# Performance work log

Measured on AMD Instinct MI355X. Metric: run time of the kernel, lower is better.

## Reference

```python
import jax, jax.numpy as jnp
import numpy as np

B, T, D = 4, 1024, 1024
NEXP, TOPK = 8, 2
N = B * T
# eval capacity: floor(TOPK * 2.0 * N / NEXP) = 2048, already even and >= min_capacity
CAP = 2048
LN_EPS = 1e-5


def setup_inputs() -> dict:
    key = jax.random.key(0)
    ks = jax.random.split(key, 4)
    x = jax.random.normal(ks[0], (B, T, D), jnp.float32)
    w_g = jax.random.normal(ks[1], (D, NEXP), jnp.float32) * 0.02
    c_fc = jax.random.normal(ks[2], (NEXP, D, 4 * D), jnp.float32) * 0.02
    c_proj = jax.random.normal(ks[3], (NEXP, 4 * D, D), jnp.float32) * 0.02
    ln_w = jnp.ones((D,), jnp.float32)
    ln_b = jnp.zeros((D,), jnp.float32)
    return {"x": x, "w_g": w_g, "c_fc": c_fc, "c_proj": c_proj, "ln_w": ln_w, "ln_b": ln_b}


def moe_forward(x, w_g, c_fc, c_proj, ln_w, ln_b):
    xf = x.reshape(N, D)
    # --- Router ---
    logits = xf @ w_g                                   # [N, E]
    topk_vals, topk_idx = jax.lax.top_k(logits, TOPK)   # [N, K]
    masked = jnp.full_like(logits, -jnp.inf)
    masked = masked.at[jnp.arange(N)[:, None], topk_idx].set(topk_vals)
    probs = jax.nn.softmax(masked, axis=-1)             # [N, E]

    # capacity-based ranking (slot 0 for all tokens first, then slot 1, ...)
    onehot = jax.nn.one_hot(topk_idx, NEXP, dtype=jnp.int32)     # [N, K, E]
    exp_mask = jnp.transpose(onehot, (1, 0, 2))                  # [K, N, E]
    rank = jnp.cumsum(exp_mask.reshape(TOPK * N, NEXP), axis=0) - 1
    rank = rank.reshape(TOPK, N, NEXP)
    exp_mask = exp_mask * (rank < CAP).astype(jnp.int32)         # drop overflow
    rank_tok = jnp.sum(exp_mask * rank, axis=-1)                 # [K, N]
    exp_w = exp_mask.astype(probs.dtype) * probs[None]           # [K, N, E]
    rank_oh = jax.nn.one_hot(rank_tok, CAP, dtype=probs.dtype)   # [K, N, C]
    cb_weight = jnp.einsum('kne,knc->nec', exp_w, rank_oh)       # [N, E, C]
    sec_mask = (cb_weight != 0).astype(x.dtype)                  # dispatch mask

    # --- dispatch -> experts -> combine ---
    xb = jnp.einsum('nec,nd->ecd', sec_mask, xf)                 # [E, C, D]
    h = jax.nn.gelu(jnp.einsum('ecd,edf->ecf', xb, c_fc), approximate=False)
    eo = jnp.einsum('ecf,efd->ecd', h, c_proj)                   # [E, C, D]
    out = jnp.einsum('nec,ecd->nd', cb_weight, eo)               # [N, D]

    # --- LayerNorm ---
    mu = out.mean(-1, keepdims=True)
    var = out.var(-1, keepdims=True)
    out = (out - mu) / jnp.sqrt(var + LN_EPS) * ln_w + ln_b
    return out.reshape(B, T, D)


def reference(x, w_g, c_fc, c_proj, ln_w, ln_b):
    return moe_forward(x, w_g, c_fc, c_proj, ln_w, ln_b)
```

## Files before the change

kernel.cpp:

```cpp
#include <hip/hip_runtime.h>
#include <math.h>

#define NEXP 8
#define CAP 2048
#define NTOK 4096
#define DDIM 1024
#define FDIM 4096

typedef __bf16 bf16x8 __attribute__((ext_vector_type(8)));
typedef float f32x4 __attribute__((ext_vector_type(4)));
typedef unsigned short u16x8 __attribute__((ext_vector_type(8)));

__device__ __forceinline__ unsigned short f2bf(float f) {
    unsigned int u = __float_as_uint(f);
    u += 0x7FFFu + ((u >> 16) & 1u);
    return (unsigned short)(u >> 16);
}

__device__ __forceinline__ void gld_lds16(const void* g, void* l) {
    __builtin_amdgcn_global_load_lds((const __attribute__((address_space(1))) void*)g,
                                     (__attribute__((address_space(3))) void*)l, 16, 0, 0);
}

__global__ __launch_bounds__(256) void transpose_cvt64(const float* __restrict__ in,
                                                       unsigned short* __restrict__ out,
                                                       int R, int C) {
    __shared__ float tile[64][65];
    int e = blockIdx.z;
    const float* ip = in + (size_t)e * R * C;
    unsigned short* op = out + (size_t)e * R * C;
    int c0 = blockIdx.x * 64, r0 = blockIdx.y * 64;
    int t = threadIdx.x;
#pragma unroll
    for (int i = 0; i < 4; i++) {
        int rr = i * 16 + (t >> 4);
        int cc = (t & 15) * 4;
        float4 v = *(const float4*)&ip[(size_t)(r0 + rr) * C + c0 + cc];
        tile[rr][cc] = v.x; tile[rr][cc + 1] = v.y; tile[rr][cc + 2] = v.z; tile[rr][cc + 3] = v.w;
    }
    __syncthreads();
    int c = t >> 2, rb = (t & 3) * 16;
    u16x8 o0, o1;
#pragma unroll
    for (int j = 0; j < 8; j++) o0[j] = f2bf(tile[rb + j][c]);
#pragma unroll
    for (int j = 0; j < 8; j++) o1[j] = f2bf(tile[rb + 8 + j][c]);
    unsigned short* dst = op + (size_t)(c0 + c) * R + r0 + rb;
    *(u16x8*)dst = o0;
    *(u16x8*)(dst + 8) = o1;
}

__global__ __launch_bounds__(256) void router_kernel(const float* __restrict__ x,
                                                     const float* __restrict__ wg,
                                                     int2* __restrict__ e01,
                                                     float2* __restrict__ p01) {
    int wid = threadIdx.x >> 6, lane = threadIdx.x & 63;
    int n = blockIdx.x * 4 + wid;
    float acc[8];
#pragma unroll
    for (int i = 0; i < 8; i++) acc[i] = 0.f;
    const float4* xr = (const float4*)(x + (size_t)n * DDIM);
#pragma unroll
    for (int j = 0; j < 4; j++) {
        float4 xv = xr[j * 64 + lane];
        int base = (j * 64 + lane) * 4;
        float xs[4] = {xv.x, xv.y, xv.z, xv.w};
#pragma unroll
        for (int t = 0; t < 4; t++) {
            const float4* wr = (const float4*)(wg + (size_t)(base + t) * 8);
            float4 w0 = wr[0], w1 = wr[1];
            acc[0] += xs[t] * w0.x; acc[1] += xs[t] * w0.y;
            acc[2] += xs[t] * w0.z; acc[3] += xs[t] * w0.w;
            acc[4] += xs[t] * w1.x; acc[5] += xs[t] * w1.y;
            acc[6] += xs[t] * w1.z; acc[7] += xs[t] * w1.w;
        }
    }
#pragma unroll
    for (int off = 32; off > 0; off >>= 1) {
#pragma unroll
        for (int i = 0; i < 8; i++) acc[i] += __shfl_xor(acc[i], off);
    }
    if (lane == 0) {
        int i0 = 0; float v0 = acc[0];
#pragma unroll
        for (int q = 1; q < 8; q++) { if (acc[q] > v0) { v0 = acc[q]; i0 = q; } }
        int i1 = -1; float v1 = -3.0e38f;
#pragma unroll
        for (int q = 0; q < 8; q++) { if (q != i0 && acc[q] > v1) { v1 = acc[q]; i1 = q; } }
        float ea = expf(v0 - v0), eb = expf(v1 - v0);
        float inv = 1.f / (ea + eb);
        e01[n] = make_int2(i0, i1);
        p01[n] = make_float2(ea * inv, eb * inv);
    }
}

__global__ void assign_kernel(const int2* __restrict__ e01, int* __restrict__ counts,
                              int* __restrict__ assign_row, int* __restrict__ tok_slot) {
    int lane = threadIdx.x;
    int base[8];
#pragma unroll
    for (int i = 0; i < 8; i++) base[i] = 0;
    unsigned long long below = ((unsigned long long)1 << lane) - 1ull;
    int2 cur = e01[lane];
    for (int pass = 0; pass < 2; ++pass) {
        for (int t = 0; t < NTOK; t += 64) {
            int n = t + lane;
            int2 nxt;
            if (t + 64 < NTOK) nxt = e01[t + 64 + lane];
            else nxt = (pass == 0) ? e01[lane] : make_int2(0, 0);
            int ex = (pass == 0) ? cur.x : cur.y;
            int slot = -1;
#pragma unroll
            for (int q = 0; q < 8; q++) {
                unsigned long long m = __ballot(ex == q);
                if (ex == q) slot = base[q] + __popcll(m & below);
                base[q] += __popcll(m);
            }
            if (slot < CAP) {
                assign_row[ex * CAP + slot] = n;
                tok_slot[2 * n + pass] = slot;
            } else {
                tok_slot[2 * n + pass] = -1;
            }
            cur = nxt;
        }
    }
    if (lane < 8) counts[lane] = base[lane] > CAP ? CAP : base[lane];
}

__global__ __launch_bounds__(256) void gather_rows(const float* __restrict__ x,
                                                   const int* __restrict__ assign_row,
                                                   const int* __restrict__ counts,
                                                   unsigned short* __restrict__ xg) {
    int e = blockIdx.y;
    int wid = threadIdx.x >> 6, lane = threadIdx.x & 63;
    int slot = blockIdx.x * 4 + wid;
    if (slot >= counts[e]) return;
    int n = assign_row[e * CAP + slot];
    const float4* src = (const float4*)(x + (size_t)n * DDIM);
    unsigned short* dst = xg + ((size_t)e * CAP + slot) * DDIM;
#pragma unroll
    for (int j = 0; j < 4; j++) {
        float4 v = src[j * 64 + lane];
        ushort4 o;
        o.x = f2bf(v.x); o.y = f2bf(v.y); o.z = f2bf(v.z); o.w = f2bf(v.w);
        *(ushort4*)(dst + (size_t)(j * 64 + lane) * 4) = o;
    }
}

template <bool GELU>
__global__ __launch_bounds__(512, 2) void gemm_pipe(const unsigned short* __restrict__ A,
                                                    const unsigned short* __restrict__ Bt,
                                                    void* __restrict__ Cout,
                                                    const int* __restrict__ counts,
                                                    int Mcap, int Ncols, int K) {
    constexpr int ABYTES = 128 * 64 * 2;
    constexpr int BBYTES = 256 * 64 * 2;
    constexpr int BUFB = ABYTES + BBYTES;
    __shared__ __align__(16) char smem[3 * BUFB];

    int gx = gridDim.x, gy = gridDim.y;
    int nwg = gx * gy * gridDim.z;
    int flat = blockIdx.x + gx * (blockIdx.y + gy * blockIdx.z);
    int cpx = nwg >> 3;
    int swz = (flat & 7) * cpx + (flat >> 3);
    int gxy = gx * gy;
    int e  = swz / gxy;
    int r2 = swz - e * gxy;
    int by = r2 / gx;
    int bx = r2 - by * gx;

    int cnt = counts[e];
    int row0 = by * 128;
    if (row0 >= cnt) return;
    int col0 = bx * 256;

    int tid = threadIdx.x;
    int w = tid >> 6, lane = tid & 63;
    int wm = w >> 2, wn = w & 3;

    const unsigned short* Ab = A + ((size_t)e * Mcap + row0) * K;
    const unsigned short* Bb = Bt + ((size_t)e * Ncols + col0) * K;
    int NT = K >> 6;

    int srow = w * 8 + (lane >> 3);
    int sElem = ((lane & 7) ^ (lane >> 3)) * 8;
    int ldst = w * 1024 + lane * 16;

    int a_off[4][2], b_off[4][2];
#pragma unroll
    for (int m = 0; m < 4; m++) {
        int row = wm * 64 + m * 16 + (lane & 15);
#pragma unroll
        for (int ks = 0; ks < 2; ks++) {
            int j = ks * 4 + (lane >> 4);
            a_off[m][ks] = row * 128 + ((j ^ (row & 7)) * 16);
        }
    }
#pragma unroll
    for (int n = 0; n < 4; n++) {
        int row = wn * 64 + n * 16 + (lane & 15);
#pragma unroll
        for (int ks = 0; ks < 2; ks++) {
            int j = ks * 4 + (lane >> 4);
            b_off[n][ks] = row * 128 + ((j ^ (row & 7)) * 16);
        }
    }

    auto stage = [&](int tt) {
        int bb = (tt % 3) * BUFB;
        size_t kq = (size_t)tt * 64 + sElem;
#pragma unroll
        for (int r = 0; r < 2; r++)
            gld_lds16(Ab + (size_t)(r * 64 + srow) * K + kq, smem + bb + r * 8192 + ldst);
#pragma unroll
        for (int r = 0; r < 4; r++)
            gld_lds16(Bb + (size_t)(r * 64 + srow) * K + kq, smem + bb + ABYTES + r * 8192 + ldst);
    };

    f32x4 acc[4][4] = {};

    stage(0); stage(1);
    asm volatile("s_waitcnt vmcnt(6)" ::: "memory");
    __builtin_amdgcn_sched_barrier(0);
    __builtin_amdgcn_s_barrier();

    for (int t = 0; t < NT; ++t) {
        const int bb = (t % 3) * BUFB;
        bf16x8 af[4][2], bf[4][2];
#pragma unroll
        for (int m = 0; m < 4; m++)
#pragma unroll
            for (int ks = 0; ks < 2; ks++)
                af[m][ks] = *(const bf16x8*)(smem + bb + a_off[m][ks]);
#pragma unroll
        for (int n = 0; n < 4; n++)
#pragma unroll
            for (int ks = 0; ks < 2; ks++)
                bf[n][ks] = *(const bf16x8*)(smem + bb + ABYTES + b_off[n][ks]);

        if (t + 2 < NT) stage(t + 2);

        if (t + 1 < NT) {
            if (t + 2 < NT) asm volatile("s_waitcnt vmcnt(6)" ::: "memory");
            else            asm volatile("s_waitcnt vmcnt(0)" ::: "memory");
        }
        __builtin_amdgcn_sched_barrier(0);
        __builtin_amdgcn_s_barrier();
        asm volatile("s_waitcnt lgkmcnt(0)" ::: "memory");
        __builtin_amdgcn_sched_barrier(0);

        __builtin_amdgcn_s_setprio(1);
#pragma unroll
        for (int ks = 0; ks < 2; ks++)
#pragma unroll
            for (int m = 0; m < 4; m++)
#pragma unroll
                for (int n = 0; n < 4; n++)
                    acc[m][n] = __builtin_amdgcn_mfma_f32_16x16x32_bf16(af[m][ks], bf[n][ks], acc[m][n], 0, 0, 0);
        __builtin_amdgcn_s_setprio(0);
        __builtin_amdgcn_s_barrier();
    }

    unsigned short* Cb_h = (unsigned short*)Cout + ((size_t)e * Mcap + row0) * Ncols + col0;
    float* Cb_f = (float*)Cout + ((size_t)e * Mcap + row0) * Ncols + col0;
#pragma unroll
    for (int m = 0; m < 4; m++)
#pragma unroll
        for (int n = 0; n < 4; n++)
#pragma unroll
            for (int j = 0; j < 4; j++) {
                int lr = wm * 64 + m * 16 + ((lane >> 4) << 2) + j;
                int lc = wn * 64 + n * 16 + (lane & 15);
                float v = acc[m][n][j];
                if constexpr (GELU) {
                    float g = 0.5f * v * (1.0f + erff(v * 0.70710678118654752f));
                    Cb_h[(size_t)lr * Ncols + lc] = f2bf(g);
                } else {
                    Cb_f[(size_t)lr * Ncols + lc] = v;
                }
            }
}

__global__ __launch_bounds__(256) void combine_ln_kernel(const float* __restrict__ eo,
                                                         const int2* __restrict__ e01,
                                                         const float2* __restrict__ p01,
                                                         const int* __restrict__ tok_slot,
                                                         const float* __restrict__ lnw,
                                                         const float* __restrict__ lnb,
                                                         float* __restrict__ out) {
    int n = blockIdx.x, t = threadIdx.x;
    int2 e = e01[n];
    float2 p = p01[n];
    int s0 = tok_slot[2 * n], s1 = tok_slot[2 * n + 1];
    float o0 = 0.f, o1 = 0.f, o2 = 0.f, o3 = 0.f;
    if (s0 >= 0) {
        const float4* r = (const float4*)(eo + ((size_t)e.x * CAP + s0) * DDIM);
        float4 v = r[t];
        o0 += p.x * v.x; o1 += p.x * v.y; o2 += p.x * v.z; o3 += p.x * v.w;
    }
    if (s1 >= 0) {
        const float4* r = (const float4*)(eo + ((size_t)e.y * CAP + s1) * DDIM);
        float4 v = r[t];
        o0 += p.y * v.x; o1 += p.y * v.y; o2 += p.y * v.z; o3 += p.y * v.w;
    }
    float s = o0 + o1 + o2 + o3;
    float sq = o0 * o0 + o1 * o1 + o2 * o2 + o3 * o3;
#pragma unroll
    for (int off = 32; off > 0; off >>= 1) {
        s += __shfl_xor(s, off);
        sq += __shfl_xor(sq, off);
    }
    __shared__ float red[8];
    int wid = t >> 6, lane = t & 63;
    if (lane == 0) { red[wid] = s; red[4 + wid] = sq; }
    __syncthreads();
    s = red[0] + red[1] + red[2] + red[3];
    sq = red[4] + red[5] + red[6] + red[7];
    float mu = s * (1.f / DDIM);
    float var = sq * (1.f / DDIM) - mu * mu;
    float inv = rsqrtf(var + 1e-5f);
    const float4 w = ((const float4*)lnw)[t];
    const float4 b = ((const float4*)lnb)[t];
    float4 r;
    r.x = (o0 - mu) * inv * w.x + b.x;
    r.y = (o1 - mu) * inv * w.y + b.y;
    r.z = (o2 - mu) * inv * w.z + b.z;
    r.w = (o3 - mu) * inv * w.w + b.w;
    ((float4*)(out + (size_t)n * DDIM))[t] = r;
}

extern "C" void kernel_launch(void* const* d_in, const int* in_sizes, int n_in,
                              void* d_out, int out_size, void* d_ws, size_t ws_size,
                              hipStream_t stream) {
    const float* x   = (const float*)d_in[0];
    const float* wg  = (const float*)d_in[1];
    const float* cfc = (const float*)d_in[2];
    const float* cpr = (const float*)d_in[3];
    const float* lnw = (const float*)d_in[4];
    const float* lnb = (const float*)d_in[5];
    float* out = (float*)d_out;

    char* ws = (char*)d_ws;
    size_t off = 0;
    auto take = [&](size_t b) {
        char* p = ws + off;
        off += (b + 255) & ~(size_t)255;
        return p;
    };
    unsigned short* cfct = (unsigned short*)take((size_t)NEXP * FDIM * DDIM * 2);
    float* eo = (float*)cfct;
    unsigned short* cprt = (unsigned short*)take((size_t)NEXP * DDIM * FDIM * 2);
    unsigned short* xg   = (unsigned short*)take((size_t)NEXP * CAP * DDIM * 2);
    unsigned short* h    = (unsigned short*)take((size_t)NEXP * CAP * FDIM * 2);
    int2*   e01      = (int2*)take(NTOK * sizeof(int2));
    float2* p01      = (float2*)take(NTOK * sizeof(float2));
    int*    tok_slot = (int*)take((size_t)NTOK * 2 * 4);
    int*    assign_row = (int*)take((size_t)NEXP * CAP * 4);
    int*    counts   = (int*)take(256);

    transpose_cvt64<<<dim3(FDIM / 64, DDIM / 64, NEXP), 256, 0, stream>>>(cfc, cfct, DDIM, FDIM);
    transpose_cvt64<<<dim3(DDIM / 64, FDIM / 64, NEXP), 256, 0, stream>>>(cpr, cprt, FDIM, DDIM);
    router_kernel<<<NTOK / 4, 256, 0, stream>>>(x, wg, e01, p01);
    assign_kernel<<<1, 64, 0, stream>>>(e01, counts, assign_row, tok_slot);
    gather_rows<<<dim3(CAP / 4, NEXP), 256, 0, stream>>>(x, assign_row, counts, xg);
    gemm_pipe<true ><<<dim3(FDIM / 256, CAP / 128, NEXP), 512, 0, stream>>>(xg, cfct, (void*)h, counts, CAP, FDIM, DDIM);
    gemm_pipe<false><<<dim3(DDIM / 256, CAP / 128, NEXP), 512, 0, stream>>>(h, cprt, (void*)eo, counts, CAP, DDIM, FDIM);
    combine_ln_kernel<<<NTOK, 256, 0, stream>>>(eo, e01, p01, tok_slot, lnw, lnb, out);
}
```

Before: 415.9 us.

## Template expert GEMM with two-phase K-step pipeline and per-GEMM tile shapes

Replaces the fixed 128x256 triple-buffered expert GEMM with a templated kernel that uses K-steps of 32, four LDS buffers, and splits each step into two half-M MFMA phases. The A and B tile loads are staged separately between the phases. The FC GEMM now uses 256x256 tiles and the projection GEMM uses 256x128 tiles. The aim is better overlap of global-to-LDS loads with MFMA work and more operand reuse per workgroup. In exchange it adds barriers per K-step, raises register and LDS pressure, and launches fewer workgroups for the FC GEMM.

```diff
diff --git a/kernel.cpp b/kernel.cpp
--- a/kernel.cpp
+++ b/kernel.cpp
@@ -148,16 +148,23 @@
     }
 }
 
-template <bool GELU>
-__global__ __launch_bounds__(512, 2) void gemm_pipe(const unsigned short* __restrict__ A,
-                                                    const unsigned short* __restrict__ Bt,
-                                                    void* __restrict__ Cout,
-                                                    const int* __restrict__ counts,
-                                                    int Mcap, int Ncols, int K) {
-    constexpr int ABYTES = 128 * 64 * 2;
-    constexpr int BBYTES = 256 * 64 * 2;
+template <int WGN, int MF, int NF, bool GELU>
+__global__ __launch_bounds__(512, 2) void gemm_2ph(const unsigned short* __restrict__ A,
+                                                   const unsigned short* __restrict__ Bt,
+                                                   void* __restrict__ Cout,
+                                                   const int* __restrict__ counts,
+                                                   int Mcap, int Ncols, int K) {
+    constexpr int WGM = 8 / WGN;
+    constexpr int BM = WGM * MF * 16;
+    constexpr int BN = WGN * NF * 16;
+    constexpr int ABYTES = BM * 64;
+    constexpr int BBYTES = BN * 64;
     constexpr int BUFB = ABYTES + BBYTES;
-    __shared__ __align__(16) char smem[3 * BUFB];
+    constexpr int GA = (BM * 4) / 512;
+    constexpr int GB = (BN * 4) / 512;
+    constexpr int LPT = GA + GB;
+    constexpr int MH = MF / 2;
+    __shared__ __align__(16) char smem[4 * BUFB];
 
     int gx = gridDim.x, gy = gridDim.y;
     int nwg = gx * gy * gridDim.z;
@@ -171,108 +178,119 @@
     int bx = r2 - by * gx;
 
     int cnt = counts[e];
-    int row0 = by * 128;
+    int row0 = by * BM;
     if (row0 >= cnt) return;
-    int col0 = bx * 256;
+    int col0 = bx * BN;
 
     int tid = threadIdx.x;
     int w = tid >> 6, lane = tid & 63;
-    int wm = w >> 2, wn = w & 3;
+    int wm = w / WGN, wn = w % WGN;
 
     const unsigned short* Ab = A + ((size_t)e * Mcap + row0) * K;
     const unsigned short* Bb = Bt + ((size_t)e * Ncols + col0) * K;
-    int NT = K >> 6;
-
-    int srow = w * 8 + (lane >> 3);
-    int sElem = ((lane & 7) ^ (lane >> 3)) * 8;
+    int NT = K >> 5;
+
+    int sAr[GA], sAk[GA], sBr[GB], sBk[GB];
+#pragma unroll
+    for (int i = 0; i < GA; i++) {
+        int c = i * 512 + tid, cp = c ^ ((c >> 4) & 3);
+        sAr[i] = cp >> 2; sAk[i] = (cp & 3) * 8;
+    }
+#pragma unroll
+    for (int i = 0; i < GB; i++) {
+        int c = i * 512 + tid, cp = c ^ ((c >> 4) & 3);
+        sBr[i] = cp >> 2; sBk[i] = (cp & 3) * 8;
+    }
     int ldst = w * 1024 + lane * 16;
 
-    int a_off[4][2], b_off[4][2];
-#pragma unroll
-    for (int m = 0; m < 4; m++) {
-        int row = wm * 64 + m * 16 + (lane & 15);
-#pragma unroll
-        for (int ks = 0; ks < 2; ks++) {
-            int j = ks * 4 + (lane >> 4);
-            a_off[m][ks] = row * 128 + ((j ^ (row & 7)) * 16);
-        }
-    }
-#pragma unroll
-    for (int n = 0; n < 4; n++) {
-        int row = wn * 64 + n * 16 + (lane & 15);
-#pragma unroll
-        for (int ks = 0; ks < 2; ks++) {
-            int j = ks * 4 + (lane >> 4);
-            b_off[n][ks] = row * 128 + ((j ^ (row & 7)) * 16);
-        }
-    }
-
-    auto stage = [&](int tt) {
-        int bb = (tt % 3) * BUFB;
-        size_t kq = (size_t)tt * 64 + sElem;
-#pragma unroll
-        for (int r = 0; r < 2; r++)
-            gld_lds16(Ab + (size_t)(r * 64 + srow) * K + kq, smem + bb + r * 8192 + ldst);
-#pragma unroll
-        for (int r = 0; r < 4; r++)
-            gld_lds16(Bb + (size_t)(r * 64 + srow) * K + kq, smem + bb + ABYTES + r * 8192 + ldst);
+    int a_off[MF], b_off[NF];
+    int j = lane >> 4;
+#pragma unroll
+    for (int m = 0; m < MF; m++) {
+        int row = wm * (MF * 16) + m * 16 + (lane & 15);
+        a_off[m] = row * 64 + ((j ^ ((row >> 2) & 3)) * 16);
+    }
+#pragma unroll
+    for (int n = 0; n < NF; n++) {
+        int row = wn * (NF * 16) + n * 16 + (lane & 15);
+        b_off[n] = row * 64 + ((j ^ ((row >> 2) & 3)) * 16);
+    }
+
+    auto stageA = [&](int tt) {
+        int bb = (tt & 3) * BUFB;
+        size_t kt = (size_t)tt * 32;
+#pragma unroll
+        for (int i = 0; i < GA; i++)
+            gld_lds16(Ab + (size_t)sAr[i] * K + kt + sAk[i], smem + bb + i * 8192 + ldst);
     };
-
-    f32x4 acc[4][4] = {};
-
-    stage(0); stage(1);
-    asm volatile("s_waitcnt vmcnt(6)" ::: "memory");
+    auto stageB = [&](int tt) {
+        int bb = (tt & 3) * BUFB + ABYTES;
+        size_t kt = (size_t)tt * 32;
+#pragma unroll
+        for (int i = 0; i < GB; i++)
+            gld_lds16(Bb + (size_t)sBr[i] * K + kt + sBk[i], smem + bb + i * 8192 + ldst);
+    };
+
+#define VM_LPT() do { if constexpr (LPT == 4) asm volatile("s_waitcnt vmcnt(4)" ::: "memory"); \
+                      else                    asm volatile("s_waitcnt vmcnt(3)" ::: "memory"); } while (0)
+
+    f32x4 acc[MF][NF] = {};
+
+    stageA(0); stageB(0); stageA(1); stageB(1);
+    VM_LPT();
     __builtin_amdgcn_sched_barrier(0);
     __builtin_amdgcn_s_barrier();
 
     for (int t = 0; t < NT; ++t) {
-        const int bb = (t % 3) * BUFB;
-        bf16x8 af[4][2], bf[4][2];
-#pragma unroll
-        for (int m = 0; m < 4; m++)
-#pragma unroll
-            for (int ks = 0; ks < 2; ks++)
-                af[m][ks] = *(const bf16x8*)(smem + bb + a_off[m][ks]);
-#pragma unroll
-        for (int n = 0; n < 4; n++)
-#pragma unroll
-            for (int ks = 0; ks < 2; ks++)
-                bf[n][ks] = *(const bf16x8*)(smem + bb + ABYTES + b_off[n][ks]);
-
-        if (t + 2 < NT) stage(t + 2);
-
-        if (t + 1 < NT) {
-            if (t + 2 < NT) asm volatile("s_waitcnt vmcnt(6)" ::: "memory");
-            else            asm volatile("s_waitcnt vmcnt(0)" ::: "memory");
-        }
+        const int bb = (t & 3) * BUFB;
+        bf16x8 af[MF], bfr[NF];
+#pragma unroll
+        for (int n = 0; n < NF; n++) bfr[n] = *(const bf16x8*)(smem + bb + ABYTES + b_off[n]);
+#pragma unroll
+        for (int m = 0; m < MH; m++) af[m] = *(const bf16x8*)(smem + bb + a_off[m]);
+        if (t + 2 < NT) stageA(t + 2);
+        __builtin_amdgcn_s_barrier();
+        asm volatile("s_waitcnt lgkmcnt(0)" ::: "memory");
+        __builtin_amdgcn_sched_barrier(0);
+        __builtin_amdgcn_s_setprio(1);
+#pragma unroll
+        for (int m = 0; m < MH; m++)
+#pragma unroll
+            for (int n = 0; n < NF; n++)
+                acc[m][n] = __builtin_amdgcn_mfma_f32_16x16x32_bf16(af[m], bfr[n], acc[m][n], 0, 0, 0);
+        __builtin_amdgcn_s_setprio(0);
+        __builtin_amdgcn_s_barrier();
+#pragma unroll
+        for (int m = MH; m < MF; m++) af[m] = *(const bf16x8*)(smem + bb + a_off[m]);
+        if (t + 2 < NT) stageB(t + 2);
+        if (t + 2 < NT)      VM_LPT();
+        else if (t + 1 < NT) asm volatile("s_waitcnt vmcnt(0)" ::: "memory");
         __builtin_amdgcn_sched_barrier(0);
         __builtin_amdgcn_s_barrier();
         asm volatile("s_waitcnt lgkmcnt(0)" ::: "memory");
         __builtin_amdgcn_sched_barrier(0);
-
         __builtin_amdgcn_s_setprio(1);
 #pragma unroll
-        for (int ks = 0; ks < 2; ks++)
-#pragma unroll
-            for (int m = 0; m < 4; m++)
-#pragma unroll
-                for (int n = 0; n < 4; n++)
-                    acc[m][n] = __builtin_amdgcn_mfma_f32_16x16x32_bf16(af[m][ks], bf[n][ks], acc[m][n], 0, 0, 0);
+        for (int m = MH; m < MF; m++)
+#pragma unroll
+            for (int n = 0; n < NF; n++)
+                acc[m][n] = __builtin_amdgcn_mfma_f32_16x16x32_bf16(af[m], bfr[n], acc[m][n], 0, 0, 0);
         __builtin_amdgcn_s_setprio(0);
         __builtin_amdgcn_s_barrier();
     }
+#undef VM_LPT
 
     unsigned short* Cb_h = (unsigned short*)Cout + ((size_t)e * Mcap + row0) * Ncols + col0;
     float* Cb_f = (float*)Cout + ((size_t)e * Mcap + row0) * Ncols + col0;
 #pragma unroll
-    for (int m = 0; m < 4; m++)
-#pragma unroll
-        for (int n = 0; n < 4; n++)
-#pragma unroll
-            for (int j = 0; j < 4; j++) {
-                int lr = wm * 64 + m * 16 + ((lane >> 4) << 2) + j;
-                int lc = wn * 64 + n * 16 + (lane & 15);
-                float v = acc[m][n][j];
+    for (int m = 0; m < MF; m++)
+#pragma unroll
+        for (int n = 0; n < NF; n++)
+#pragma unroll
+            for (int jj = 0; jj < 4; jj++) {
+                int lr = wm * (MF * 16) + m * 16 + ((lane >> 4) << 2) + jj;
+                int lc = wn * (NF * 16) + n * 16 + (lane & 15);
+                float v = acc[m][n][jj];
                 if constexpr (GELU) {
                     float g = 0.5f * v * (1.0f + erff(v * 0.70710678118654752f));
                     Cb_h[(size_t)lr * Ncols + lc] = f2bf(g);
@@ -364,7 +382,7 @@
     router_kernel<<<NTOK / 4, 256, 0, stream>>>(x, wg, e01, p01);
     assign_kernel<<<1, 64, 0, stream>>>(e01, counts, assign_row, tok_slot);
     gather_rows<<<dim3(CAP / 4, NEXP), 256, 0, stream>>>(x, assign_row, counts, xg);
-    gemm_pipe<true ><<<dim3(FDIM / 256, CAP / 128, NEXP), 512, 0, stream>>>(xg, cfct, (void*)h, counts, CAP, FDIM, DDIM);
-    gemm_pipe<false><<<dim3(DDIM / 256, CAP / 128, NEXP), 512, 0, stream>>>(h, cprt, (void*)eo, counts, CAP, DDIM, FDIM);
+    gemm_2ph<4, 8, 4, true ><<<dim3(FDIM / 256, CAP / 256, NEXP), 512, 0, stream>>>(xg, cfct, (void*)h, counts, CAP, FDIM, DDIM);
+    gemm_2ph<2, 4, 4, false><<<dim3(DDIM / 128, CAP / 256, NEXP), 512, 0, stream>>>(h, cprt, (void*)eo, counts, CAP, DDIM, FDIM);
     combine_ln_kernel<<<NTOK, 256, 0, stream>>>(eo, e01, p01, tok_slot, lnw, lnb, out);
 }
```

After: 443.9 us. 6.7% more time.

## Replace triple-buffered K64 GEMM with templated double-buffered K32 GEMM

Applied to the files above, without the earlier changes.

Swaps the 3-stage, 64-wide-K pipelined expert GEMM for a templated double-buffered kernel that uses 32-wide K tiles, a new LDS swizzle and a plain __syncthreads per iteration. The template lets the second GEMM run with 128x128 tiles and 256 threads, which gives more workgroups for the narrow N=1024 output. Launch bounds are raised to 4 waves per EU, trading pipeline depth for occupancy. The cost is a barrier every 32 K, half the MFMA work between barriers, and the loss of the explicit vmcnt-based overlap.

```diff
diff --git a/kernel.cpp b/kernel.cpp
--- a/kernel.cpp
+++ b/kernel.cpp
@@ -148,16 +148,21 @@
     }
 }
 
-template <bool GELU>
-__global__ __launch_bounds__(512, 2) void gemm_pipe(const unsigned short* __restrict__ A,
-                                                    const unsigned short* __restrict__ Bt,
-                                                    void* __restrict__ Cout,
-                                                    const int* __restrict__ counts,
-                                                    int Mcap, int Ncols, int K) {
-    constexpr int ABYTES = 128 * 64 * 2;
-    constexpr int BBYTES = 256 * 64 * 2;
+template <int WM, int WN, bool GELU>
+__global__ __launch_bounds__(WM * WN * 64, 4) void gemm_db(const unsigned short* __restrict__ A,
+                                                           const unsigned short* __restrict__ Bt,
+                                                           void* __restrict__ Cout,
+                                                           const int* __restrict__ counts,
+                                                           int Mcap, int Ncols, int K) {
+    constexpr int T = WM * WN * 64;
+    constexpr int BM = WM * 64;
+    constexpr int BN = WN * 64;
+    constexpr int ABYTES = BM * 64;
+    constexpr int BBYTES = BN * 64;
     constexpr int BUFB = ABYTES + BBYTES;
-    __shared__ __align__(16) char smem[3 * BUFB];
+    constexpr int GA = (BM * 4) / T;
+    constexpr int GB = (BN * 4) / T;
+    __shared__ __align__(16) char smem[2 * BUFB];
 
     int gx = gridDim.x, gy = gridDim.y;
     int nwg = gx * gy * gridDim.z;
@@ -171,95 +176,69 @@
     int bx = r2 - by * gx;
 
     int cnt = counts[e];
-    int row0 = by * 128;
+    int row0 = by * BM;
     if (row0 >= cnt) return;
-    int col0 = bx * 256;
+    int col0 = bx * BN;
 
     int tid = threadIdx.x;
     int w = tid >> 6, lane = tid & 63;
-    int wm = w >> 2, wn = w & 3;
+    int wm = w / WN, wn = w % WN;
 
     const unsigned short* Ab = A + ((size_t)e * Mcap + row0) * K;
     const unsigned short* Bb = Bt + ((size_t)e * Ncols + col0) * K;
-    int NT = K >> 6;
-
-    int srow = w * 8 + (lane >> 3);
-    int sElem = ((lane & 7) ^ (lane >> 3)) * 8;
-    int ldst = w * 1024 + lane * 16;
-
-    int a_off[4][2], b_off[4][2];
+    int NT = K >> 5;
+
+    int kel = (((tid & 3) ^ ((tid >> 3) & 3)) * 8);
+    int rA = tid >> 2;
+    int ldst = tid * 16;
+
+    int a_off[4], b_off[4];
+    int c = lane >> 4;
 #pragma unroll
     for (int m = 0; m < 4; m++) {
         int row = wm * 64 + m * 16 + (lane & 15);
-#pragma unroll
-        for (int ks = 0; ks < 2; ks++) {
-            int j = ks * 4 + (lane >> 4);
-            a_off[m][ks] = row * 128 + ((j ^ (row & 7)) * 16);
-        }
+        a_off[m] = row * 64 + ((c ^ ((row >> 1) & 3)) * 16);
     }
 #pragma unroll
     for (int n = 0; n < 4; n++) {
         int row = wn * 64 + n * 16 + (lane & 15);
-#pragma unroll
-        for (int ks = 0; ks < 2; ks++) {
-            int j = ks * 4 + (lane >> 4);
-            b_off[n][ks] = row * 128 + ((j ^ (row & 7)) * 16);
-        }
+        b_off[n] = row * 64 + ((c ^ ((row >> 1) & 3)) * 16);
     }
 
     auto stage = [&](int tt) {
-        int bb = (tt % 3) * BUFB;
-        size_t kq = (size_t)tt * 64 + sElem;
-#pragma unroll
-        for (int r = 0; r < 2; r++)
-            gld_lds16(Ab + (size_t)(r * 64 + srow) * K + kq, smem + bb + r * 8192 + ldst);
-#pragma unroll
-        for (int r = 0; r < 4; r++)
-            gld_lds16(Bb + (size_t)(r * 64 + srow) * K + kq, smem + bb + ABYTES + r * 8192 + ldst);
+        int bb = (tt & 1) * BUFB;
+        size_t kt = (size_t)tt * 32 + kel;
+#pragma unroll
+        for (int i = 0; i < GA; i++)
+            gld_lds16(Ab + (size_t)(i * (T / 4) + rA) * K + kt, smem + bb + i * T * 16 + ldst);
+#pragma unroll
+        for (int i = 0; i < GB; i++)
+            gld_lds16(Bb + (size_t)(i * (T / 4) + rA) * K + kt, smem + bb + ABYTES + i * T * 16 + ldst);
     };
 
     f32x4 acc[4][4] = {};
 
-    stage(0); stage(1);
-    asm volatile("s_waitcnt vmcnt(6)" ::: "memory");
+    stage(0);
     __builtin_amdgcn_sched_barrier(0);
-    __builtin_amdgcn_s_barrier();
+    __syncthreads();
 
     for (int t = 0; t < NT; ++t) {
-        const int bb = (t % 3) * BUFB;
-        bf16x8 af[4][2], bf[4][2];
+        const int bb = (t & 1) * BUFB;
+        if (t + 1 < NT) stage(t + 1);
+        __builtin_amdgcn_sched_barrier(0);
+        bf16x8 af[4], bfr[4];
+#pragma unroll
+        for (int m = 0; m < 4; m++) af[m] = *(const bf16x8*)(smem + bb + a_off[m]);
+#pragma unroll
+        for (int n = 0; n < 4; n++) bfr[n] = *(const bf16x8*)(smem + bb + ABYTES + b_off[n]);
+        __builtin_amdgcn_s_setprio(1);
 #pragma unroll
         for (int m = 0; m < 4; m++)
 #pragma unroll
-            for (int ks = 0; ks < 2; ks++)
-                af[m][ks] = *(const bf16x8*)(smem + bb + a_off[m][ks]);
-#pragma unroll
-        for (int n = 0; n < 4; n++)
-#pragma unroll
-            for (int ks = 0; ks < 2; ks++)
-                bf[n][ks] = *(const bf16x8*)(smem + bb + ABYTES + b_off[n][ks]);
-
-        if (t + 2 < NT) stage(t + 2);
-
-        if (t + 1 < NT) {
-            if (t + 2 < NT) asm volatile("s_waitcnt vmcnt(6)" ::: "memory");
-            else            asm volatile("s_waitcnt vmcnt(0)" ::: "memory");
-        }
-        __builtin_amdgcn_sched_barrier(0);
-        __builtin_amdgcn_s_barrier();
-        asm volatile("s_waitcnt lgkmcnt(0)" ::: "memory");
-        __builtin_amdgcn_sched_barrier(0);
-
-        __builtin_amdgcn_s_setprio(1);
-#pragma unroll
-        for (int ks = 0; ks < 2; ks++)
-#pragma unroll
-            for (int m = 0; m < 4; m++)
-#pragma unroll
-                for (int n = 0; n < 4; n++)
-                    acc[m][n] = __builtin_amdgcn_mfma_f32_16x16x32_bf16(af[m][ks], bf[n][ks], acc[m][n], 0, 0, 0);
+            for (int n = 0; n < 4; n++)
+                acc[m][n] = __builtin_amdgcn_mfma_f32_16x16x32_bf16(af[m], bfr[n], acc[m][n], 0, 0, 0);
         __builtin_amdgcn_s_setprio(0);
-        __builtin_amdgcn_s_barrier();
+        __syncthreads();
     }
 
     unsigned short* Cb_h = (unsigned short*)Cout + ((size_t)e * Mcap + row0) * Ncols + col0;
@@ -364,7 +343,7 @@
     router_kernel<<<NTOK / 4, 256, 0, stream>>>(x, wg, e01, p01);
     assign_kernel<<<1, 64, 0, stream>>>(e01, counts, assign_row, tok_slot);
     gather_rows<<<dim3(CAP / 4, NEXP), 256, 0, stream>>>(x, assign_row, counts, xg);
-    gemm_pipe<true ><<<dim3(FDIM / 256, CAP / 128, NEXP), 512, 0, stream>>>(xg, cfct, (void*)h, counts, CAP, FDIM, DDIM);
-    gemm_pipe<false><<<dim3(DDIM / 256, CAP / 128, NEXP), 512, 0, stream>>>(h, cprt, (void*)eo, counts, CAP, DDIM, FDIM);
+    gemm_db<2, 4, true ><<<dim3(FDIM / 256, CAP / 128, NEXP), 512, 0, stream>>>(xg, cfct, (void*)h, counts, CAP, FDIM, DDIM);
+    gemm_db<2, 2, false><<<dim3(DDIM / 128, CAP / 128, NEXP), 256, 0, stream>>>(h, cprt, (void*)eo, counts, CAP, DDIM, FDIM);
     combine_ln_kernel<<<NTOK, 256, 0, stream>>>(eo, e01, p01, tok_slot, lnw, lnb, out);
 }
```

Measured after the change: 357.5 us. 14.0% less time.

## Use 256x256 GEMM tiles with 8-phase half-K pipelining and split-K for down-projection

Applied to the files above, without the earlier changes.

The GEMM kernel moves from 128x256 tiles with a triple-buffered 64-wide K pipeline to 256x256 tiles. Each K step is split into half-tile loads interleaved with four MFMA phases, using 128KB of LDS for double buffering. The second GEMM is split-K by 2, writing two bf16 partial planes that the combine/LayerNorm kernel sums. This is meant to raise arithmetic intensity per tile and fill the GPU better for the smaller projection GEMM, at the cost of bf16 rounding of expert outputs, more LDS per workgroup and more register pressure.

```diff
diff --git a/kernel.cpp b/kernel.cpp
--- a/kernel.cpp
+++ b/kernel.cpp
@@ -15,6 +15,9 @@
     unsigned int u = __float_as_uint(f);
     u += 0x7FFFu + ((u >> 16) & 1u);
     return (unsigned short)(u >> 16);
+}
+__device__ __forceinline__ float bf2f(unsigned short h) {
+    return __uint_as_float(((unsigned int)h) << 16);
 }
 
 __device__ __forceinline__ void gld_lds16(const void* g, void* l) {
@@ -148,16 +151,13 @@
     }
 }
 
-template <bool GELU>
-__global__ __launch_bounds__(512, 2) void gemm_pipe(const unsigned short* __restrict__ A,
-                                                    const unsigned short* __restrict__ Bt,
-                                                    void* __restrict__ Cout,
-                                                    const int* __restrict__ counts,
-                                                    int Mcap, int Ncols, int K) {
-    constexpr int ABYTES = 128 * 64 * 2;
-    constexpr int BBYTES = 256 * 64 * 2;
-    constexpr int BUFB = ABYTES + BBYTES;
-    __shared__ __align__(16) char smem[3 * BUFB];
+template <bool GELU, int KC>
+__global__ __launch_bounds__(512, 2) void gemm_8ph(const unsigned short* __restrict__ A,
+                                                   const unsigned short* __restrict__ Bt,
+                                                   unsigned short* __restrict__ Cout,
+                                                   const int* __restrict__ counts,
+                                                   int Ncols, int Ktot) {
+    __shared__ __align__(16) char smem[131072];
 
     int gx = gridDim.x, gy = gridDim.y;
     int nwg = gx * gy * gridDim.z;
@@ -165,144 +165,189 @@
     int cpx = nwg >> 3;
     int swz = (flat & 7) * cpx + (flat >> 3);
     int gxy = gx * gy;
-    int e  = swz / gxy;
-    int r2 = swz - e * gxy;
+    int zz = swz / gxy;
+    int r2 = swz - zz * gxy;
     int by = r2 / gx;
     int bx = r2 - by * gx;
+    int e = zz / KC, kc = zz % KC;
 
     int cnt = counts[e];
-    int row0 = by * 128;
+    int row0 = by * 256;
     if (row0 >= cnt) return;
     int col0 = bx * 256;
-
-    int tid = threadIdx.x;
-    int w = tid >> 6, lane = tid & 63;
+    const int Ksub = Ktot / KC;
+    const int NT = Ksub >> 6;
+
+    const unsigned short* Ab = A + ((size_t)e * CAP + row0) * Ktot + (size_t)kc * Ksub;
+    const unsigned short* Bb = Bt + ((size_t)e * Ncols + col0) * Ktot + (size_t)kc * Ksub;
+
+    int tid = threadIdx.x, w = tid >> 6, lane = tid & 63;
     int wm = w >> 2, wn = w & 3;
 
-    const unsigned short* Ab = A + ((size_t)e * Mcap + row0) * K;
-    const unsigned short* Bb = Bt + ((size_t)e * Ncols + col0) * K;
-    int NT = K >> 6;
-
-    int srow = w * 8 + (lane >> 3);
-    int sElem = ((lane & 7) ^ (lane >> 3)) * 8;
-    int ldst = w * 1024 + lane * 16;
-
-    int a_off[4][2], b_off[4][2];
-#pragma unroll
-    for (int m = 0; m < 4; m++) {
-        int row = wm * 64 + m * 16 + (lane & 15);
-#pragma unroll
-        for (int ks = 0; ks < 2; ks++) {
-            int j = ks * 4 + (lane >> 4);
-            a_off[m][ks] = row * 128 + ((j ^ (row & 7)) * 16);
-        }
-    }
-#pragma unroll
-    for (int n = 0; n < 4; n++) {
-        int row = wn * 64 + n * 16 + (lane & 15);
-#pragma unroll
-        for (int ks = 0; ks < 2; ks++) {
-            int j = ks * 4 + (lane >> 4);
-            b_off[n][ks] = row * 128 + ((j ^ (row & 7)) * 16);
-        }
-    }
-
-    auto stage = [&](int tt) {
-        int bb = (tt % 3) * BUFB;
-        size_t kq = (size_t)tt * 64 + sElem;
-#pragma unroll
-        for (int r = 0; r < 2; r++)
-            gld_lds16(Ab + (size_t)(r * 64 + srow) * K + kq, smem + bb + r * 8192 + ldst);
-#pragma unroll
-        for (int r = 0; r < 4; r++)
-            gld_lds16(Bb + (size_t)(r * 64 + srow) * K + kq, smem + bb + ABYTES + r * 8192 + ldst);
+    int kel = (((tid & 3) ^ ((tid >> 3) & 3)) * 8);
+
+    int aoff[8], boff[4];
+    int c0 = lane >> 4;
+#pragma unroll
+    for (int mq = 0; mq < 8; mq++) {
+        int row = wm * 128 + mq * 16 + (lane & 15);
+        aoff[mq] = row * 64 + ((c0 ^ ((row >> 1) & 3)) << 4);
+    }
+#pragma unroll
+    for (int nq = 0; nq < 4; nq++) {
+        int row = wn * 64 + nq * 16 + (lane & 15);
+        boff[nq] = row * 64 + ((c0 ^ ((row >> 1) & 3)) << 4);
+    }
+
+    auto stage_half = [&](int hidx) {
+        int tau = hidx >> 2, h = hidx & 3;
+        const unsigned short* src = (h & 1) ? Bb : Ab;
+        char* base = smem + ((h & 1) ? 65536 : 0) + (((tau & 1) << 1) + (h >> 1)) * 16384;
+        size_t kq = (size_t)tau * 64 + ((h >> 1) << 5) + kel;
+#pragma unroll
+        for (int i = 0; i < 2; i++)
+            gld_lds16(src + (size_t)(i * 128 + (tid >> 2)) * Ktot + kq,
+                      base + i * 8192 + tid * 16);
     };
 
-    f32x4 acc[4][4] = {};
-
-    stage(0); stage(1);
-    asm volatile("s_waitcnt vmcnt(6)" ::: "memory");
+    f32x4 acc[8][4] = {};
+
+#pragma unroll
+    for (int hh = 0; hh < 6; ++hh) stage_half(hh);
+    asm volatile("s_waitcnt vmcnt(4)" ::: "memory");
     __builtin_amdgcn_sched_barrier(0);
     __builtin_amdgcn_s_barrier();
 
+    const int H = 4 * NT;
     for (int t = 0; t < NT; ++t) {
-        const int bb = (t % 3) * BUFB;
-        bf16x8 af[4][2], bf[4][2];
+        const int db = t & 1;
+        const char* A0 = smem + (db * 2 + 0) * 16384;
+        const char* A1 = smem + (db * 2 + 1) * 16384;
+        const char* B0 = smem + 65536 + (db * 2 + 0) * 16384;
+        const char* B1 = smem + 65536 + (db * 2 + 1) * 16384;
+        const int h6 = 4 * t + 6;
+        bf16x8 a[4], b[4];
+
+#pragma unroll
+        for (int n = 0; n < 4; n++) b[n] = *(const bf16x8*)(B0 + boff[n]);
+#pragma unroll
+        for (int m = 0; m < 4; m++) a[m] = *(const bf16x8*)(A0 + aoff[m]);
+        if (h6 + 0 < H) stage_half(h6 + 0);
+        __builtin_amdgcn_sched_barrier(0);
+        __builtin_amdgcn_s_barrier();
+        asm volatile("s_waitcnt lgkmcnt(0)" ::: "memory");
+        __builtin_amdgcn_sched_barrier(0);
+        __builtin_amdgcn_s_setprio(1);
 #pragma unroll
         for (int m = 0; m < 4; m++)
 #pragma unroll
-            for (int ks = 0; ks < 2; ks++)
-                af[m][ks] = *(const bf16x8*)(smem + bb + a_off[m][ks]);
+            for (int n = 0; n < 4; n++)
+                acc[m][n] = __builtin_amdgcn_mfma_f32_16x16x32_bf16(a[m], b[n], acc[m][n], 0, 0, 0);
+        __builtin_amdgcn_s_setprio(0);
+        __builtin_amdgcn_s_barrier();
+
+#pragma unroll
+        for (int m = 0; m < 4; m++) a[m] = *(const bf16x8*)(A0 + aoff[4 + m]);
+        if (h6 + 1 < H) stage_half(h6 + 1);
+        __builtin_amdgcn_sched_barrier(0);
+        __builtin_amdgcn_s_barrier();
+        asm volatile("s_waitcnt lgkmcnt(0)" ::: "memory");
+        __builtin_amdgcn_sched_barrier(0);
+        __builtin_amdgcn_s_setprio(1);
+#pragma unroll
+        for (int m = 0; m < 4; m++)
+#pragma unroll
+            for (int n = 0; n < 4; n++)
+                acc[4 + m][n] = __builtin_amdgcn_mfma_f32_16x16x32_bf16(a[m], b[n], acc[4 + m][n], 0, 0, 0);
+        __builtin_amdgcn_s_setprio(0);
+        __builtin_amdgcn_s_barrier();
+
+#pragma unroll
+        for (int n = 0; n < 4; n++) b[n] = *(const bf16x8*)(B1 + boff[n]);
+#pragma unroll
+        for (int m = 0; m < 4; m++) a[m] = *(const bf16x8*)(A1 + aoff[m]);
+        if (h6 + 2 < H) stage_half(h6 + 2);
+        __builtin_amdgcn_sched_barrier(0);
+        __builtin_amdgcn_s_barrier();
+        asm volatile("s_waitcnt lgkmcnt(0)" ::: "memory");
+        __builtin_amdgcn_sched_barrier(0);
+        __builtin_amdgcn_s_setprio(1);
+#pragma unroll
+        for (int m = 0; m < 4; m++)
+#pragma unroll
+            for (int n = 0; n < 4; n++)
+                acc[m][n] = __builtin_amdgcn_mfma_f32_16x16x32_bf16(a[m], b[n], acc[m][n], 0, 0, 0);
+        __builtin_amdgcn_s_setprio(0);
+        __builtin_amdgcn_s_barrier();
+
+#pragma unroll
+        for (int m = 0; m < 4; m++) a[m] = *(const bf16x8*)(A1 + aoff[4 + m]);
+        if (h6 + 3 < H) stage_half(h6 + 3);
+        if (t + 2 < NT)      asm volatile("s_waitcnt vmcnt(4)" ::: "memory");
+        else if (t + 1 < NT) asm volatile("s_waitcnt vmcnt(0)" ::: "memory");
+        __builtin_amdgcn_sched_barrier(0);
+        __builtin_amdgcn_s_barrier();
+        asm volatile("s_waitcnt lgkmcnt(0)" ::: "memory");
+        __builtin_amdgcn_sched_barrier(0);
+        __builtin_amdgcn_s_setprio(1);
+#pragma unroll
+        for (int m = 0; m < 4; m++)
+#pragma unroll
+            for (int n = 0; n < 4; n++)
+                acc[4 + m][n] = __builtin_amdgcn_mfma_f32_16x16x32_bf16(a[m], b[n], acc[4 + m][n], 0, 0, 0);
+        __builtin_amdgcn_s_setprio(0);
+        __builtin_amdgcn_s_barrier();
+    }
+
+    unsigned short* Cb = Cout + (((size_t)(kc * NEXP + e) * CAP + row0)) * Ncols + col0;
+#pragma unroll
+    for (int mq = 0; mq < 8; mq++)
 #pragma unroll
         for (int n = 0; n < 4; n++)
 #pragma unroll
-            for (int ks = 0; ks < 2; ks++)
-                bf[n][ks] = *(const bf16x8*)(smem + bb + ABYTES + b_off[n][ks]);
-
-        if (t + 2 < NT) stage(t + 2);
-
-        if (t + 1 < NT) {
-            if (t + 2 < NT) asm volatile("s_waitcnt vmcnt(6)" ::: "memory");
-            else            asm volatile("s_waitcnt vmcnt(0)" ::: "memory");
-        }
-        __builtin_amdgcn_sched_barrier(0);
-        __builtin_amdgcn_s_barrier();
-        asm volatile("s_waitcnt lgkmcnt(0)" ::: "memory");
-        __builtin_amdgcn_sched_barrier(0);
-
-        __builtin_amdgcn_s_setprio(1);
-#pragma unroll
-        for (int ks = 0; ks < 2; ks++)
-#pragma unroll
-            for (int m = 0; m < 4; m++)
-#pragma unroll
-                for (int n = 0; n < 4; n++)
-                    acc[m][n] = __builtin_amdgcn_mfma_f32_16x16x32_bf16(af[m][ks], bf[n][ks], acc[m][n], 0, 0, 0);
-        __builtin_amdgcn_s_setprio(0);
-        __builtin_amdgcn_s_barrier();
-    }
-
-    unsigned short* Cb_h = (unsigned short*)Cout + ((size_t)e * Mcap + row0) * Ncols + col0;
-    float* Cb_f = (float*)Cout + ((size_t)e * Mcap + row0) * Ncols + col0;
-#pragma unroll
-    for (int m = 0; m < 4; m++)
-#pragma unroll
-        for (int n = 0; n < 4; n++)
-#pragma unroll
             for (int j = 0; j < 4; j++) {
-                int lr = wm * 64 + m * 16 + ((lane >> 4) << 2) + j;
+                int lr = wm * 128 + mq * 16 + ((lane >> 4) << 2) + j;
                 int lc = wn * 64 + n * 16 + (lane & 15);
-                float v = acc[m][n][j];
+                float v = acc[mq][n][j];
                 if constexpr (GELU) {
                     float g = 0.5f * v * (1.0f + erff(v * 0.70710678118654752f));
-                    Cb_h[(size_t)lr * Ncols + lc] = f2bf(g);
+                    Cb[(size_t)lr * Ncols + lc] = f2bf(g);
                 } else {
-                    Cb_f[(size_t)lr * Ncols + lc] = v;
+                    Cb[(size_t)lr * Ncols + lc] = f2bf(v);
                 }
             }
 }
 
-__global__ __launch_bounds__(256) void combine_ln_kernel(const float* __restrict__ eo,
+__global__ __launch_bounds__(256) void combine_ln_kernel(const unsigned short* __restrict__ pb,
                                                          const int2* __restrict__ e01,
                                                          const float2* __restrict__ p01,
                                                          const int* __restrict__ tok_slot,
                                                          const float* __restrict__ lnw,
                                                          const float* __restrict__ lnb,
                                                          float* __restrict__ out) {
+    const size_t PLANE = (size_t)NEXP * CAP * DDIM;
     int n = blockIdx.x, t = threadIdx.x;
     int2 e = e01[n];
     float2 p = p01[n];
     int s0 = tok_slot[2 * n], s1 = tok_slot[2 * n + 1];
     float o0 = 0.f, o1 = 0.f, o2 = 0.f, o3 = 0.f;
     if (s0 >= 0) {
-        const float4* r = (const float4*)(eo + ((size_t)e.x * CAP + s0) * DDIM);
-        float4 v = r[t];
-        o0 += p.x * v.x; o1 += p.x * v.y; o2 += p.x * v.z; o3 += p.x * v.w;
+        size_t base = ((size_t)e.x * CAP + s0) * DDIM;
+        ushort4 u0 = ((const ushort4*)(pb + base))[t];
+        ushort4 u1 = ((const ushort4*)(pb + PLANE + base))[t];
+        o0 += p.x * (bf2f(u0.x) + bf2f(u1.x));
+        o1 += p.x * (bf2f(u0.y) + bf2f(u1.y));
+        o2 += p.x * (bf2f(u0.z) + bf2f(u1.z));
+        o3 += p.x * (bf2f(u0.w) + bf2f(u1.w));
     }
     if (s1 >= 0) {
-        const float4* r = (const float4*)(eo + ((size_t)e.y * CAP + s1) * DDIM);
-        float4 v = r[t];
-        o0 += p.y * v.x; o1 += p.y * v.y; o2 += p.y * v.z; o3 += p.y * v.w;
+        size_t base = ((size_t)e.y * CAP + s1) * DDIM;
+        ushort4 u0 = ((const ushort4*)(pb + base))[t];
+        ushort4 u1 = ((const ushort4*)(pb + PLANE + base))[t];
+        o0 += p.y * (bf2f(u0.x) + bf2f(u1.x));
+        o1 += p.y * (bf2f(u0.y) + bf2f(u1.y));
+        o2 += p.y * (bf2f(u0.z) + bf2f(u1.z));
+        o3 += p.y * (bf2f(u0.w) + bf2f(u1.w));
     }
     float s = o0 + o1 + o2 + o3;
     float sq = o0 * o0 + o1 * o1 + o2 * o2 + o3 * o3;
@@ -349,7 +394,7 @@
         return p;
     };
     unsigned short* cfct = (unsigned short*)take((size_t)NEXP * FDIM * DDIM * 2);
-    float* eo = (float*)cfct;
+    unsigned short* pb = cfct;
     unsigned short* cprt = (unsigned short*)take((size_t)NEXP * DDIM * FDIM * 2);
     unsigned short* xg   = (unsigned short*)take((size_t)NEXP * CAP * DDIM * 2);
     unsigned short* h    = (unsigned short*)take((size_t)NEXP * CAP * FDIM * 2);
@@ -364,7 +409,7 @@
     router_kernel<<<NTOK / 4, 256, 0, stream>>>(x, wg, e01, p01);
     assign_kernel<<<1, 64, 0, stream>>>(e01, counts, assign_row, tok_slot);
     gather_rows<<<dim3(CAP / 4, NEXP), 256, 0, stream>>>(x, assign_row, counts, xg);
-    gemm_pipe<true ><<<dim3(FDIM / 256, CAP / 128, NEXP), 512, 0, stream>>>(xg, cfct, (void*)h, counts, CAP, FDIM, DDIM);
-    gemm_pipe<false><<<dim3(DDIM / 256, CAP / 128, NEXP), 512, 0, stream>>>(h, cprt, (void*)eo, counts, CAP, DDIM, FDIM);
-    combine_ln_kernel<<<NTOK, 256, 0, stream>>>(eo, e01, p01, tok_slot, lnw, lnb, out);
-}
+    gemm_8ph<true, 1><<<dim3(FDIM / 256, CAP / 256, NEXP), 512, 0, stream>>>(xg, cfct, h, counts, FDIM, DDIM);
+    gemm_8ph<false, 2><<<dim3(DDIM / 256, CAP / 256, NEXP * 2), 512, 0, stream>>>(h, cprt, pb, counts, DDIM, FDIM);
+    combine_ln_kernel<<<NTOK, 256, 0, stream>>>(pb, e01, p01, tok_slot, lnw, lnb, out);
+}
```

Result: no change. 411.6 us (-1.0%).
